# Performance work log

Hardware: AMD Instinct MI355X
Metric: run time of the kernel (lower is better)

## Reference

```python
import jax, jax.numpy as jnp
import numpy as np

N = 500000        # total atoms (n1 nodes)
G = 20000         # graphs (g nodes)
D_IN = 128        # in_features
D_H = 256         # hidden width (config_local / mid_features)
D_OUT = 1         # final output per graph (config_global last int)


def setup_inputs() -> dict:
    key = jax.random.key(0)
    ks = jax.random.split(key, 10)
    h = jax.random.normal(ks[0], (N, D_IN), dtype=jnp.float32)
    graph_ids = jnp.sort(jax.random.randint(ks[1], (N,), 0, G))
    s = 0.05
    return {
        "h": h,
        "graph_ids": graph_ids,
        "num_graphs": G,
        # d_local: Linear(128->256) relu, Linear(256->256) relu
        "W1": jax.random.normal(ks[2], (D_IN, D_H), dtype=jnp.float32) * s,
        "b1": jnp.zeros((D_H,), dtype=jnp.float32),
        "W2": jax.random.normal(ks[3], (D_H, D_H), dtype=jnp.float32) * s,
        "b2": jnp.zeros((D_H,), dtype=jnp.float32),
        # d_global: Linear(256->256) relu, Linear(256->1)
        "Wg1": jax.random.normal(ks[4], (D_H, D_H), dtype=jnp.float32) * s,
        "bg1": jnp.zeros((D_H,), dtype=jnp.float32),
        "Wg2": jax.random.normal(ks[5], (D_H, D_OUT), dtype=jnp.float32) * s,
        "bg2": jnp.zeros((D_OUT,), dtype=jnp.float32),
    }


def reference(h, graph_ids, num_graphs, W1, b1, W2, b2, Wg1, bg1, Wg2, bg2):
    # node-level MLP (d_local): h_global per n1 node
    x = jax.nn.relu(h @ W1 + b1)            # [N, D_H]
    x = jax.nn.relu(x @ W2 + b2)            # [N, D_H]
    # copy_src + sum over n1_in_g edges == per-graph segment sum
    pooled = jax.ops.segment_sum(x, graph_ids, num_segments=num_graphs)  # [G, D_H]
    # graph-level MLP (d_global)
    y = jax.nn.relu(pooled @ Wg1 + bg1)     # [G, D_H]
    return y @ Wg2 + bg2                    # [G, 1]
```

## Files before the change

### kernel.cpp

```cpp
#include <hip/hip_runtime.h>
#include <stdint.h>

#define D_IN 128
#define D_H  256
#define BM   64

typedef float f32x4 __attribute__((ext_vector_type(4)));
typedef short s16x8 __attribute__((ext_vector_type(8)));
typedef unsigned int u32x2 __attribute__((ext_vector_type(2)));
typedef unsigned int u32x4 __attribute__((ext_vector_type(4)));

__device__ __forceinline__ unsigned short f2bf(float x) {
  union { float f; uint32_t u; } v; v.f = x;
  uint32_t r = v.u + 0x7fffu + ((v.u >> 16) & 1u);
  return (unsigned short)(r >> 16);
}
__device__ __forceinline__ float bf2f(unsigned short u) {
  union { uint32_t u; float f; } v; v.u = (uint32_t)u << 16;
  return v.f;
}

__global__ void prep_kernel(const float* __restrict__ W1, const float* __restrict__ W2,
                            const float* __restrict__ Wg1,
                            float* __restrict__ pooled, unsigned short* __restrict__ W1t,
                            unsigned short* __restrict__ W2t, unsigned short* __restrict__ Wg1t,
                            int pooled_n) {
  int stride = gridDim.x * blockDim.x;
  int tid = blockIdx.x * blockDim.x + threadIdx.x;
  for (int i = tid; i < pooled_n; i += stride) pooled[i] = 0.0f;
  for (int i = tid; i < D_H * D_IN; i += stride) {
    int n = i >> 7, k = i & (D_IN - 1);
    W1t[i] = f2bf(W1[k * D_H + n]);
  }
  for (int i = tid; i < D_H * D_H; i += stride) {
    int n = i >> 8, k = i & (D_H - 1);
    W2t[i]  = f2bf(W2[k * D_H + n]);
    Wg1t[i] = f2bf(Wg1[k * D_H + n]);
  }
}


__global__ __launch_bounds__(256, 3)
void node_kernel(const float* __restrict__ h, const int* __restrict__ gids,
                 const float* __restrict__ b1, const float* __restrict__ b2,
                 const unsigned short* __restrict__ W1t, const unsigned short* __restrict__ W2t,
                 float* __restrict__ pooled, int nnodes) {
  __shared__ unsigned short hA[BM * D_IN];
  __shared__ unsigned short x1s[BM * D_H];
  __shared__ int sgid[BM];
  const int tid  = threadIdx.x;
  const int lane = tid & 63;
  const int wave = tid >> 6;
  const int lr   = lane & 15;
  const int q    = lane >> 4;
  const int row0 = blockIdx.x * BM;

  s16x8 a[4][4];
  #pragma unroll
  for (int ks = 0; ks < 4; ++ks)
    #pragma unroll
    for (int mt = 0; mt < 4; ++mt)
      a[ks][mt] = *(const s16x8*)&W1t[(wave * 64 + mt * 16 + lr) * D_IN + ks * 32 + q * 8];

  if (tid < BM) {
    int gr = row0 + tid;
    sgid[tid] = (gr < nnodes) ? gids[gr] : -1;
  }

  #pragma unroll
  for (int i = 0; i < 4; ++i) {
    int gi = tid + i * 256;
    int r  = gi >> 4;
    int gc = gi & 15;
    int gr = row0 + r;
    f32x4 v0 = (f32x4){0.f, 0.f, 0.f, 0.f}, v1 = v0;
    if (gr < nnodes) {
      const f32x4* p = (const f32x4*)(h + (size_t)gr * D_IN + gc * 8);
      v0 = __builtin_nontemporal_load(p);
      v1 = __builtin_nontemporal_load(p + 1);
    }
    u32x4 u;
    u[0] = f2bf(v0[0]) | ((uint32_t)f2bf(v0[1]) << 16);
    u[1] = f2bf(v0[2]) | ((uint32_t)f2bf(v0[3]) << 16);
    u[2] = f2bf(v1[0]) | ((uint32_t)f2bf(v1[1]) << 16);
    u[3] = f2bf(v1[2]) | ((uint32_t)f2bf(v1[3]) << 16);
    *(u32x4*)&hA[r * D_IN + ((gc ^ (r & 7)) << 3)] = u;
  }
  __syncthreads();

  f32x4 acc[4][4];
  #pragma unroll
  for (int mt = 0; mt < 4; ++mt)
    #pragma unroll
    for (int nt = 0; nt < 4; ++nt)
      acc[mt][nt] = (f32x4){0.f, 0.f, 0.f, 0.f};

  #pragma unroll
  for (int ks = 0; ks < 4; ++ks) {
    const int kq = ks * 32 + q * 8;
    s16x8 b[4];
    #pragma unroll
    for (int nt = 0; nt < 4; ++nt)
      b[nt] = *(const s16x8*)&hA[(nt * 16 + lr) * D_IN + (((kq >> 3) ^ (lr & 7)) << 3)];
    #pragma unroll
    for (int mt = 0; mt < 4; ++mt)
      #pragma unroll
      for (int nt = 0; nt < 4; ++nt)
        acc[mt][nt] = __builtin_amdgcn_mfma_f32_16x16x32_bf16(a[ks][mt], b[nt], acc[mt][nt], 0, 0, 0);
  }

  #pragma unroll
  for (int mt = 0; mt < 4; ++mt) {
    int f = wave * 64 + mt * 16 + q * 4;
    float4 bias = *(const float4*)&b1[f];
    #pragma unroll
    for (int nt = 0; nt < 4; ++nt) {
      int nd = nt * 16 + lr;
      uint32_t p0 = f2bf(fmaxf(acc[mt][nt][0] + bias.x, 0.f)) |
                    ((uint32_t)f2bf(fmaxf(acc[mt][nt][1] + bias.y, 0.f)) << 16);
      uint32_t p1 = f2bf(fmaxf(acc[mt][nt][2] + bias.z, 0.f)) |
                    ((uint32_t)f2bf(fmaxf(acc[mt][nt][3] + bias.w, 0.f)) << 16);
      u32x2 w = {p0, p1};
      *(u32x2*)&x1s[nd * D_H + (((f >> 3) ^ (nd & 7)) << 3) + (f & 7)] = w;
    }
  }

  #pragma unroll
  for (int ks = 0; ks < 4; ++ks)
    #pragma unroll
    for (int mt = 0; mt < 4; ++mt)
      a[ks][mt] = *(const s16x8*)&W2t[(wave * 64 + mt * 16 + lr) * D_H + ks * 32 + q * 8];
  __syncthreads();

  #pragma unroll
  for (int mt = 0; mt < 4; ++mt)
    #pragma unroll
    for (int nt = 0; nt < 4; ++nt)
      acc[mt][nt] = (f32x4){0.f, 0.f, 0.f, 0.f};

  #pragma unroll
  for (int ks = 0; ks < 4; ++ks) {
    const int kq = ks * 32 + q * 8;
    s16x8 b[4];
    #pragma unroll
    for (int nt = 0; nt < 4; ++nt)
      b[nt] = *(const s16x8*)&x1s[(nt * 16 + lr) * D_H + (((kq >> 3) ^ (lr & 7)) << 3)];
    #pragma unroll
    for (int mt = 0; mt < 4; ++mt)
      #pragma unroll
      for (int nt = 0; nt < 4; ++nt)
        acc[mt][nt] = __builtin_amdgcn_mfma_f32_16x16x32_bf16(a[ks][mt], b[nt], acc[mt][nt], 0, 0, 0);
  }
  #pragma unroll
  for (int ks = 0; ks < 4; ++ks)
    #pragma unroll
    for (int mt = 0; mt < 4; ++mt)
      a[ks][mt] = *(const s16x8*)&W2t[(wave * 64 + mt * 16 + lr) * D_H + 128 + ks * 32 + q * 8];
  #pragma unroll
  for (int ks = 0; ks < 4; ++ks) {
    const int kq = 128 + ks * 32 + q * 8;
    s16x8 b[4];
    #pragma unroll
    for (int nt = 0; nt < 4; ++nt)
      b[nt] = *(const s16x8*)&x1s[(nt * 16 + lr) * D_H + (((kq >> 3) ^ (lr & 7)) << 3)];
    #pragma unroll
    for (int mt = 0; mt < 4; ++mt)
      #pragma unroll
      for (int nt = 0; nt < 4; ++nt)
        acc[mt][nt] = __builtin_amdgcn_mfma_f32_16x16x32_bf16(a[ks][mt], b[nt], acc[mt][nt], 0, 0, 0);
  }
  __syncthreads();

  #pragma unroll
  for (int mt = 0; mt < 4; ++mt) {
    int f = wave * 64 + mt * 16 + q * 4;
    float4 bias = *(const float4*)&b2[f];
    #pragma unroll
    for (int nt = 0; nt < 4; ++nt) {
      int nd = nt * 16 + lr;
      uint32_t p0 = f2bf(fmaxf(acc[mt][nt][0] + bias.x, 0.f)) |
                    ((uint32_t)f2bf(fmaxf(acc[mt][nt][1] + bias.y, 0.f)) << 16);
      uint32_t p1 = f2bf(fmaxf(acc[mt][nt][2] + bias.z, 0.f)) |
                    ((uint32_t)f2bf(fmaxf(acc[mt][nt][3] + bias.w, 0.f)) << 16);
      u32x2 w = {p0, p1};
      *(u32x2*)&x1s[nd * D_H + (((f >> 3) ^ (nd & 7)) << 3) + (f & 7)] = w;
    }
  }
  __syncthreads();

  float racc = 0.f;
  for (int r = 0; r < BM; ++r) {
    int g = sgid[r];
    if (g >= 0) {
      racc += bf2f(x1s[r * D_H + (((tid >> 3) ^ (r & 7)) << 3) + (tid & 7)]);
      if (r == BM - 1 || sgid[r + 1] != g) {
        atomicAdd(&pooled[g * D_H + tid], racc);
        racc = 0.f;
      }
    }
  }
}

union GraphSmem {
  unsigned short pA[BM][D_H + 8];
  float y[BM][D_H + 4];
};

__global__ __launch_bounds__(256, 2)
void graph_kernel(const float* __restrict__ pooled, const float* __restrict__ bg1,
                  const unsigned short* __restrict__ Wg1t, const float* __restrict__ Wg2,
                  const float* __restrict__ bg2, float* __restrict__ out, int ngraphs) {
  __shared__ GraphSmem sm;
  const int tid  = threadIdx.x;
  const int lane = tid & 63;
  const int wave = tid >> 6;
  const int lr   = lane & 15;
  const int q    = lane >> 4;
  const int g0   = blockIdx.x * BM;

  #pragma unroll
  for (int i = 0; i < 16; ++i) {
    int f4 = tid + i * 256;
    int r  = f4 >> 6;
    int c4 = f4 & 63;
    float4 v = make_float4(0.f, 0.f, 0.f, 0.f);
    if (g0 + r < ngraphs) v = ((const float4*)pooled)[(size_t)(g0 + r) * 64 + c4];
    uint32_t p0 = f2bf(v.x) | ((uint32_t)f2bf(v.y) << 16);
    uint32_t p1 = f2bf(v.z) | ((uint32_t)f2bf(v.w) << 16);
    uint32_t* dst = (uint32_t*)&sm.pA[r][c4 * 4];
    dst[0] = p0; dst[1] = p1;
  }
  __syncthreads();

  f32x4 acc[4][4];
  #pragma unroll
  for (int mt = 0; mt < 4; ++mt)
    #pragma unroll
    for (int nt = 0; nt < 4; ++nt)
      acc[mt][nt] = (f32x4){0.f, 0.f, 0.f, 0.f};

  #pragma unroll
  for (int kk = 0; kk < D_H; kk += 32) {
    const int kq = kk + q * 8;
    s16x8 a[4], b[4];
    #pragma unroll
    for (int mt = 0; mt < 4; ++mt) {
      int f = wave * 64 + mt * 16 + lr;
      a[mt] = *(const s16x8*)&Wg1t[f * D_H + kq];
    }
    #pragma unroll
    for (int nt = 0; nt < 4; ++nt)
      b[nt] = *(const s16x8*)&sm.pA[nt * 16 + lr][kq];
    #pragma unroll
    for (int mt = 0; mt < 4; ++mt)
      #pragma unroll
      for (int nt = 0; nt < 4; ++nt)
        acc[mt][nt] = __builtin_amdgcn_mfma_f32_16x16x32_bf16(a[mt], b[nt], acc[mt][nt], 0, 0, 0);
  }
  __syncthreads();

  #pragma unroll
  for (int mt = 0; mt < 4; ++mt) {
    int f = wave * 64 + mt * 16 + q * 4;
    float4 bias = *(const float4*)&bg1[f];
    #pragma unroll
    for (int nt = 0; nt < 4; ++nt) {
      int nd = nt * 16 + lr;
      f32x4 v;
      v[0] = fmaxf(acc[mt][nt][0] + bias.x, 0.f);
      v[1] = fmaxf(acc[mt][nt][1] + bias.y, 0.f);
      v[2] = fmaxf(acc[mt][nt][2] + bias.z, 0.f);
      v[3] = fmaxf(acc[mt][nt][3] + bias.w, 0.f);
      *(f32x4*)&sm.y[nd][f] = v;
    }
  }
  __syncthreads();

  int gloc = tid >> 2;
  int part = tid & 3;
  float p = 0.f;
  #pragma unroll 8
  for (int i = 0; i < 64; ++i) {
    int f = part + 4 * i;
    p += sm.y[gloc][f] * Wg2[f];
  }
  p += __shfl_xor(p, 1);
  p += __shfl_xor(p, 2);
  if (part == 0 && (g0 + gloc) < ngraphs)
    out[g0 + gloc] = p + bg2[0];
}

extern "C" void kernel_launch(void* const* d_in, const int* in_sizes, int n_in,
                              void* d_out, int out_size, void* d_ws, size_t ws_size,
                              hipStream_t stream) {
  const float* h   = (const float*)d_in[0];
  const int*   gid = (const int*)d_in[1];
  const float* W1  = (const float*)d_in[3];
  const float* b1  = (const float*)d_in[4];
  const float* W2  = (const float*)d_in[5];
  const float* b2  = (const float*)d_in[6];
  const float* Wg1 = (const float*)d_in[7];
  const float* bg1 = (const float*)d_in[8];
  const float* Wg2 = (const float*)d_in[9];
  const float* bg2 = (const float*)d_in[10];
  float* out = (float*)d_out;

  const int N = in_sizes[1];
  const int G = out_size;

  char* ws = (char*)d_ws;
  float* pooled = (float*)ws;
  size_t off = (size_t)G * D_H * sizeof(float);
  unsigned short* W1t  = (unsigned short*)(ws + off); off += (size_t)D_H * D_IN * 2;
  unsigned short* W2t  = (unsigned short*)(ws + off); off += (size_t)D_H * D_H * 2;
  unsigned short* Wg1t = (unsigned short*)(ws + off);

  prep_kernel<<<512, 256, 0, stream>>>(W1, W2, Wg1, pooled, W1t, W2t, Wg1t, G * D_H);
  node_kernel<<<(N + BM - 1) / BM, 256, 0, stream>>>(h, gid, b1, b2, W1t, W2t, pooled, N);
  graph_kernel<<<(G + BM - 1) / BM, 256, 0, stream>>>(pooled, bg1, Wg1t, Wg2, bg2, out, G);
}
```

Before: 579.3 us.

## Make node kernel persistent with double-buffered prefetch of next tile

The node MLP kernel becomes a persistent grid of fixed size that loops over tiles. W1 fragments and biases stay in registers across tiles, and the next tile's h rows and graph ids are prefetched into registers and written to a second LDS buffer while the current tile computes. W2 fragments are streamed in halves to limit register pressure. The graph kernel keeps its intermediate in swizzled bf16 LDS instead of an fp32 union, which allows higher occupancy. The cost is more registers and a lower occupancy bound (2 blocks) for the node kernel, plus bf16 rounding of the graph hidden layer.

```diff
diff --git a/kernel.cpp b/kernel.cpp
--- a/kernel.cpp
+++ b/kernel.cpp
@@ -4,6 +4,7 @@
 #define D_IN 128
 #define D_H  256
 #define BM   64
+#define NODE_GRID 2048
 
 typedef float f32x4 __attribute__((ext_vector_type(4)));
 typedef short s16x8 __attribute__((ext_vector_type(8)));
@@ -27,7 +28,8 @@
                             int pooled_n) {
   int stride = gridDim.x * blockDim.x;
   int tid = blockIdx.x * blockDim.x + threadIdx.x;
-  for (int i = tid; i < pooled_n; i += stride) pooled[i] = 0.0f;
+  float4 z4 = make_float4(0.f, 0.f, 0.f, 0.f);
+  for (int i = tid; i < (pooled_n >> 2); i += stride) ((float4*)pooled)[i] = z4;
   for (int i = tid; i < D_H * D_IN; i += stride) {
     int n = i >> 7, k = i & (D_IN - 1);
     W1t[i] = f2bf(W1[k * D_H + n]);
@@ -39,52 +41,249 @@
   }
 }
 
-
-__global__ __launch_bounds__(256, 3)
+__global__ __launch_bounds__(256, 2)
 void node_kernel(const float* __restrict__ h, const int* __restrict__ gids,
                  const float* __restrict__ b1, const float* __restrict__ b2,
                  const unsigned short* __restrict__ W1t, const unsigned short* __restrict__ W2t,
-                 float* __restrict__ pooled, int nnodes) {
-  __shared__ unsigned short hA[BM * D_IN];
+                 float* __restrict__ pooled, int nnodes, int ntiles) {
+  __shared__ unsigned short hA[2][BM * D_IN];
   __shared__ unsigned short x1s[BM * D_H];
-  __shared__ int sgid[BM];
+  __shared__ int sgid[2][BM];
   const int tid  = threadIdx.x;
   const int lane = tid & 63;
   const int wave = tid >> 6;
   const int lr   = lane & 15;
   const int q    = lane >> 4;
-  const int row0 = blockIdx.x * BM;
-
-  s16x8 a[4][4];
+
+  if (blockIdx.x >= ntiles) return;
+
+  s16x8 a1[4][4];
   #pragma unroll
   for (int ks = 0; ks < 4; ++ks)
     #pragma unroll
     for (int mt = 0; mt < 4; ++mt)
-      a[ks][mt] = *(const s16x8*)&W1t[(wave * 64 + mt * 16 + lr) * D_IN + ks * 32 + q * 8];
-
-  if (tid < BM) {
-    int gr = row0 + tid;
-    sgid[tid] = (gr < nnodes) ? gids[gr] : -1;
-  }
-
-  #pragma unroll
-  for (int i = 0; i < 4; ++i) {
-    int gi = tid + i * 256;
-    int r  = gi >> 4;
-    int gc = gi & 15;
-    int gr = row0 + r;
+      a1[ks][mt] = *(const s16x8*)&W1t[(wave * 64 + mt * 16 + lr) * D_IN + ks * 32 + q * 8];
+  float4 b1v[4], b2v[4];
+  #pragma unroll
+  for (int mt = 0; mt < 4; ++mt) {
+    b1v[mt] = *(const float4*)&b1[wave * 64 + mt * 16 + q * 4];
+    b2v[mt] = *(const float4*)&b2[wave * 64 + mt * 16 + q * 4];
+  }
+
+  int tile = blockIdx.x;
+
+  {
+    const int row0 = tile * BM;
+    #pragma unroll
+    for (int i = 0; i < 4; ++i) {
+      int gi = tid + i * 256, r = gi >> 4, gc = gi & 15, gr = row0 + r;
+      f32x4 v0 = (f32x4){0.f, 0.f, 0.f, 0.f}, v1 = v0;
+      if (gr < nnodes) {
+        const f32x4* p = (const f32x4*)(h + (size_t)gr * D_IN + gc * 8);
+        v0 = __builtin_nontemporal_load(p);
+        v1 = __builtin_nontemporal_load(p + 1);
+      }
+      u32x4 u;
+      u[0] = f2bf(v0[0]) | ((uint32_t)f2bf(v0[1]) << 16);
+      u[1] = f2bf(v0[2]) | ((uint32_t)f2bf(v0[3]) << 16);
+      u[2] = f2bf(v1[0]) | ((uint32_t)f2bf(v1[1]) << 16);
+      u[3] = f2bf(v1[2]) | ((uint32_t)f2bf(v1[3]) << 16);
+      *(u32x4*)&hA[0][r * D_IN + ((gc ^ (r & 7)) << 3)] = u;
+    }
+    if (tid < BM) {
+      int gr = row0 + tid;
+      sgid[0][tid] = (gr < nnodes) ? gids[gr] : -1;
+    }
+  }
+  __syncthreads();
+
+  auto body = [&](int cur) {
+    const int nxt = cur ^ 1;
+    const int ntile = tile + NODE_GRID;
+    const bool has_next = ntile < ntiles;
+    const int nrow0 = ntile * BM;
+
+    f32x4 hv[8];
+    #pragma unroll
+    for (int i = 0; i < 4; ++i) {
+      int gi = tid + i * 256, r = gi >> 4, gc = gi & 15;
+      int gr = nrow0 + r;
+      hv[2 * i] = (f32x4){0.f, 0.f, 0.f, 0.f};
+      hv[2 * i + 1] = hv[2 * i];
+      if (has_next && gr < nnodes) {
+        const f32x4* p = (const f32x4*)(h + (size_t)gr * D_IN + gc * 8);
+        hv[2 * i]     = __builtin_nontemporal_load(p);
+        hv[2 * i + 1] = __builtin_nontemporal_load(p + 1);
+      }
+    }
+    int gv = -1;
+    if (has_next && tid < BM) {
+      int gr = nrow0 + tid;
+      gv = (gr < nnodes) ? gids[gr] : -1;
+    }
+
+    f32x4 acc[4][4];
+    #pragma unroll
+    for (int mt = 0; mt < 4; ++mt)
+      #pragma unroll
+      for (int nt = 0; nt < 4; ++nt)
+        acc[mt][nt] = (f32x4){0.f, 0.f, 0.f, 0.f};
+
+    #pragma unroll
+    for (int ks = 0; ks < 4; ++ks) {
+      const int kq = ks * 32 + q * 8;
+      s16x8 b[4];
+      #pragma unroll
+      for (int nt = 0; nt < 4; ++nt)
+        b[nt] = *(const s16x8*)&hA[cur][(nt * 16 + lr) * D_IN + (((kq >> 3) ^ (lr & 7)) << 3)];
+      #pragma unroll
+      for (int mt = 0; mt < 4; ++mt)
+        #pragma unroll
+        for (int nt = 0; nt < 4; ++nt)
+          acc[mt][nt] = __builtin_amdgcn_mfma_f32_16x16x32_bf16(a1[ks][mt], b[nt], acc[mt][nt], 0, 0, 0);
+    }
+
+    #pragma unroll
+    for (int mt = 0; mt < 4; ++mt) {
+      int f = wave * 64 + mt * 16 + q * 4;
+      #pragma unroll
+      for (int nt = 0; nt < 4; ++nt) {
+        int nd = nt * 16 + lr;
+        uint32_t p0 = f2bf(fmaxf(acc[mt][nt][0] + b1v[mt].x, 0.f)) |
+                      ((uint32_t)f2bf(fmaxf(acc[mt][nt][1] + b1v[mt].y, 0.f)) << 16);
+        uint32_t p1 = f2bf(fmaxf(acc[mt][nt][2] + b1v[mt].z, 0.f)) |
+                      ((uint32_t)f2bf(fmaxf(acc[mt][nt][3] + b1v[mt].w, 0.f)) << 16);
+        u32x2 w = {p0, p1};
+        *(u32x2*)&x1s[nd * D_H + (((f >> 3) ^ (nd & 7)) << 3) + (f & 7)] = w;
+      }
+    }
+
+    if (has_next) {
+      #pragma unroll
+      for (int i = 0; i < 4; ++i) {
+        int gi = tid + i * 256, r = gi >> 4, gc = gi & 15;
+        u32x4 u;
+        u[0] = f2bf(hv[2 * i][0]) | ((uint32_t)f2bf(hv[2 * i][1]) << 16);
+        u[1] = f2bf(hv[2 * i][2]) | ((uint32_t)f2bf(hv[2 * i][3]) << 16);
+        u[2] = f2bf(hv[2 * i + 1][0]) | ((uint32_t)f2bf(hv[2 * i + 1][1]) << 16);
+        u[3] = f2bf(hv[2 * i + 1][2]) | ((uint32_t)f2bf(hv[2 * i + 1][3]) << 16);
+        *(u32x4*)&hA[nxt][r * D_IN + ((gc ^ (r & 7)) << 3)] = u;
+      }
+    }
+
+    s16x8 w2[2][2][4];
+    #pragma unroll
+    for (int qq = 0; qq < 2; ++qq)
+      #pragma unroll
+      for (int ki = 0; ki < 2; ++ki)
+        #pragma unroll
+        for (int mt = 0; mt < 4; ++mt)
+          w2[qq][ki][mt] = *(const s16x8*)&W2t[(wave * 64 + mt * 16 + lr) * D_H +
+                                               ((qq * 2 + ki) * 32 + q * 8)];
+
+    __syncthreads();
+
+    #pragma unroll
+    for (int mt = 0; mt < 4; ++mt)
+      #pragma unroll
+      for (int nt = 0; nt < 4; ++nt)
+        acc[mt][nt] = (f32x4){0.f, 0.f, 0.f, 0.f};
+
+    #pragma unroll
+    for (int qq = 0; qq < 4; ++qq) {
+      const int buf = qq & 1;
+      #pragma unroll
+      for (int ki = 0; ki < 2; ++ki) {
+        const int kq = (qq * 2 + ki) * 32 + q * 8;
+        s16x8 b[4];
+        #pragma unroll
+        for (int nt = 0; nt < 4; ++nt)
+          b[nt] = *(const s16x8*)&x1s[(nt * 16 + lr) * D_H + (((kq >> 3) ^ (lr & 7)) << 3)];
+        #pragma unroll
+        for (int mt = 0; mt < 4; ++mt)
+          #pragma unroll
+          for (int nt = 0; nt < 4; ++nt)
+            acc[mt][nt] = __builtin_amdgcn_mfma_f32_16x16x32_bf16(w2[buf][ki][mt], b[nt], acc[mt][nt], 0, 0, 0);
+      }
+      if (qq < 2) {
+        #pragma unroll
+        for (int ki = 0; ki < 2; ++ki)
+          #pragma unroll
+          for (int mt = 0; mt < 4; ++mt)
+            w2[buf][ki][mt] = *(const s16x8*)&W2t[(wave * 64 + mt * 16 + lr) * D_H +
+                                                  (((qq + 2) * 2 + ki) * 32 + q * 8)];
+      }
+    }
+
+    __syncthreads();
+
+    if (has_next && tid < BM) sgid[nxt][tid] = gv;
+
+    #pragma unroll
+    for (int mt = 0; mt < 4; ++mt) {
+      int f = wave * 64 + mt * 16 + q * 4;
+      #pragma unroll
+      for (int nt = 0; nt < 4; ++nt) {
+        int nd = nt * 16 + lr;
+        uint32_t p0 = f2bf(fmaxf(acc[mt][nt][0] + b2v[mt].x, 0.f)) |
+                      ((uint32_t)f2bf(fmaxf(acc[mt][nt][1] + b2v[mt].y, 0.f)) << 16);
+        uint32_t p1 = f2bf(fmaxf(acc[mt][nt][2] + b2v[mt].z, 0.f)) |
+                      ((uint32_t)f2bf(fmaxf(acc[mt][nt][3] + b2v[mt].w, 0.f)) << 16);
+        u32x2 w = {p0, p1};
+        *(u32x2*)&x1s[nd * D_H + (((f >> 3) ^ (nd & 7)) << 3) + (f & 7)] = w;
+      }
+    }
+
+    float racc = 0.f;
+    for (int r = 0; r < BM; ++r) {
+      int g = sgid[cur][r];
+      if (g >= 0) {
+        racc += bf2f(x1s[r * D_H + (((tid >> 3) ^ (r & 7)) << 3) + (tid & 7)]);
+        if (r == BM - 1 || sgid[cur][r + 1] != g) {
+          atomicAdd(&pooled[g * D_H + tid], racc);
+          racc = 0.f;
+        }
+      }
+    }
+  };
+
+  while (true) {
+    body(0);
+    tile += NODE_GRID;
+    if (tile >= ntiles) break;
+    body(1);
+    tile += NODE_GRID;
+    if (tile >= ntiles) break;
+  }
+}
+
+__global__ __launch_bounds__(256, 4)
+void graph_kernel(const float* __restrict__ pooled, const float* __restrict__ bg1,
+                  const unsigned short* __restrict__ Wg1t, const float* __restrict__ Wg2,
+                  const float* __restrict__ bg2, float* __restrict__ out, int ngraphs) {
+  __shared__ unsigned short pA[BM * D_H];
+  const int tid  = threadIdx.x;
+  const int lane = tid & 63;
+  const int wave = tid >> 6;
+  const int lr   = lane & 15;
+  const int q    = lane >> 4;
+  const int g0   = blockIdx.x * BM;
+
+  #pragma unroll
+  for (int i = 0; i < 8; ++i) {
+    int gi = tid + i * 256, r = gi >> 5, gc = gi & 31;
+    int gr = g0 + r;
     f32x4 v0 = (f32x4){0.f, 0.f, 0.f, 0.f}, v1 = v0;
-    if (gr < nnodes) {
-      const f32x4* p = (const f32x4*)(h + (size_t)gr * D_IN + gc * 8);
-      v0 = __builtin_nontemporal_load(p);
-      v1 = __builtin_nontemporal_load(p + 1);
+    if (gr < ngraphs) {
+      const f32x4* p = (const f32x4*)(pooled + (size_t)gr * D_H + gc * 8);
+      v0 = p[0]; v1 = p[1];
     }
     u32x4 u;
     u[0] = f2bf(v0[0]) | ((uint32_t)f2bf(v0[1]) << 16);
     u[1] = f2bf(v0[2]) | ((uint32_t)f2bf(v0[3]) << 16);
     u[2] = f2bf(v1[0]) | ((uint32_t)f2bf(v1[1]) << 16);
     u[3] = f2bf(v1[2]) | ((uint32_t)f2bf(v1[3]) << 16);
-    *(u32x4*)&hA[r * D_IN + ((gc ^ (r & 7)) << 3)] = u;
+    *(u32x4*)&pA[r * D_H + (((gc & 7) ^ (r & 7)) << 3) + ((gc & 24) << 3)] = u;
   }
   __syncthreads();
 
@@ -96,23 +295,29 @@
       acc[mt][nt] = (f32x4){0.f, 0.f, 0.f, 0.f};
 
   #pragma unroll
-  for (int ks = 0; ks < 4; ++ks) {
+  for (int ks = 0; ks < 8; ++ks) {
     const int kq = ks * 32 + q * 8;
-    s16x8 b[4];
-    #pragma unroll
-    for (int nt = 0; nt < 4; ++nt)
-      b[nt] = *(const s16x8*)&hA[(nt * 16 + lr) * D_IN + (((kq >> 3) ^ (lr & 7)) << 3)];
+    s16x8 a[4], b[4];
+    #pragma unroll
+    for (int mt = 0; mt < 4; ++mt)
+      a[mt] = *(const s16x8*)&Wg1t[(wave * 64 + mt * 16 + lr) * D_H + kq];
+    #pragma unroll
+    for (int nt = 0; nt < 4; ++nt) {
+      int row = nt * 16 + lr, gw = kq >> 3;
+      b[nt] = *(const s16x8*)&pA[row * D_H + (((gw & 7) ^ (row & 7)) << 3) + ((gw & 24) << 3)];
+    }
     #pragma unroll
     for (int mt = 0; mt < 4; ++mt)
       #pragma unroll
       for (int nt = 0; nt < 4; ++nt)
-        acc[mt][nt] = __builtin_amdgcn_mfma_f32_16x16x32_bf16(a[ks][mt], b[nt], acc[mt][nt], 0, 0, 0);
-  }
+        acc[mt][nt] = __builtin_amdgcn_mfma_f32_16x16x32_bf16(a[mt], b[nt], acc[mt][nt], 0, 0, 0);
+  }
+  __syncthreads();
 
   #pragma unroll
   for (int mt = 0; mt < 4; ++mt) {
     int f = wave * 64 + mt * 16 + q * 4;
-    float4 bias = *(const float4*)&b1[f];
+    float4 bias = *(const float4*)&bg1[f];
     #pragma unroll
     for (int nt = 0; nt < 4; ++nt) {
       int nd = nt * 16 + lr;
@@ -121,157 +326,8 @@
       uint32_t p1 = f2bf(fmaxf(acc[mt][nt][2] + bias.z, 0.f)) |
                     ((uint32_t)f2bf(fmaxf(acc[mt][nt][3] + bias.w, 0.f)) << 16);
       u32x2 w = {p0, p1};
-      *(u32x2*)&x1s[nd * D_H + (((f >> 3) ^ (nd & 7)) << 3) + (f & 7)] = w;
-    }
-  }
-
-  #pragma unroll
-  for (int ks = 0; ks < 4; ++ks)
-    #pragma unroll
-    for (int mt = 0; mt < 4; ++mt)
-      a[ks][mt] = *(const s16x8*)&W2t[(wave * 64 + mt * 16 + lr) * D_H + ks * 32 + q * 8];
-  __syncthreads();
-
-  #pragma unroll
-  for (int mt = 0; mt < 4; ++mt)
-    #pragma unroll
-    for (int nt = 0; nt < 4; ++nt)
-      acc[mt][nt] = (f32x4){0.f, 0.f, 0.f, 0.f};
-
-  #pragma unroll
-  for (int ks = 0; ks < 4; ++ks) {
-    const int kq = ks * 32 + q * 8;
-    s16x8 b[4];
-    #pragma unroll
-    for (int nt = 0; nt < 4; ++nt)
-      b[nt] = *(const s16x8*)&x1s[(nt * 16 + lr) * D_H + (((kq >> 3) ^ (lr & 7)) << 3)];
-    #pragma unroll
-    for (int mt = 0; mt < 4; ++mt)
-      #pragma unroll
-      for (int nt = 0; nt < 4; ++nt)
-        acc[mt][nt] = __builtin_amdgcn_mfma_f32_16x16x32_bf16(a[ks][mt], b[nt], acc[mt][nt], 0, 0, 0);
-  }
-  #pragma unroll
-  for (int ks = 0; ks < 4; ++ks)
-    #pragma unroll
-    for (int mt = 0; mt < 4; ++mt)
-      a[ks][mt] = *(const s16x8*)&W2t[(wave * 64 + mt * 16 + lr) * D_H + 128 + ks * 32 + q * 8];
-  #pragma unroll
-  for (int ks = 0; ks < 4; ++ks) {
-    const int kq = 128 + ks * 32 + q * 8;
-    s16x8 b[4];
-    #pragma unroll
-    for (int nt = 0; nt < 4; ++nt)
-      b[nt] = *(const s16x8*)&x1s[(nt * 16 + lr) * D_H + (((kq >> 3) ^ (lr & 7)) << 3)];
-    #pragma unroll
-    for (int mt = 0; mt < 4; ++mt)
-      #pragma unroll
-      for (int nt = 0; nt < 4; ++nt)
-        acc[mt][nt] = __builtin_amdgcn_mfma_f32_16x16x32_bf16(a[ks][mt], b[nt], acc[mt][nt], 0, 0, 0);
-  }
-  __syncthreads();
-
-  #pragma unroll
-  for (int mt = 0; mt < 4; ++mt) {
-    int f = wave * 64 + mt * 16 + q * 4;
-    float4 bias = *(const float4*)&b2[f];
-    #pragma unroll
-    for (int nt = 0; nt < 4; ++nt) {
-      int nd = nt * 16 + lr;
-      uint32_t p0 = f2bf(fmaxf(acc[mt][nt][0] + bias.x, 0.f)) |
-                    ((uint32_t)f2bf(fmaxf(acc[mt][nt][1] + bias.y, 0.f)) << 16);
-      uint32_t p1 = f2bf(fmaxf(acc[mt][nt][2] + bias.z, 0.f)) |
-                    ((uint32_t)f2bf(fmaxf(acc[mt][nt][3] + bias.w, 0.f)) << 16);
-      u32x2 w = {p0, p1};
-      *(u32x2*)&x1s[nd * D_H + (((f >> 3) ^ (nd & 7)) << 3) + (f & 7)] = w;
-    }
-  }
-  __syncthreads();
-
-  float racc = 0.f;
-  for (int r = 0; r < BM; ++r) {
-    int g = sgid[r];
-    if (g >= 0) {
-      racc += bf2f(x1s[r * D_H + (((tid >> 3) ^ (r & 7)) << 3) + (tid & 7)]);
-      if (r == BM - 1 || sgid[r + 1] != g) {
-        atomicAdd(&pooled[g * D_H + tid], racc);
-        racc = 0.f;
-      }
-    }
-  }
-}
-
-union GraphSmem {
-  unsigned short pA[BM][D_H + 8];
-  float y[BM][D_H + 4];
-};
-
-__global__ __launch_bounds__(256, 2)
-void graph_kernel(const float* __restrict__ pooled, const float* __restrict__ bg1,
-                  const unsigned short* __restrict__ Wg1t, const float* __restrict__ Wg2,
-                  const float* __restrict__ bg2, float* __restrict__ out, int ngraphs) {
-  __shared__ GraphSmem sm;
-  const int tid  = threadIdx.x;
-  const int lane = tid & 63;
-  const int wave = tid >> 6;
-  const int lr   = lane & 15;
-  const int q    = lane >> 4;
-  const int g0   = blockIdx.x * BM;
-
-  #pragma unroll
-  for (int i = 0; i < 16; ++i) {
-    int f4 = tid + i * 256;
-    int r  = f4 >> 6;
-    int c4 = f4 & 63;
-    float4 v = make_float4(0.f, 0.f, 0.f, 0.f);
-    if (g0 + r < ngraphs) v = ((const float4*)pooled)[(size_t)(g0 + r) * 64 + c4];
-    uint32_t p0 = f2bf(v.x) | ((uint32_t)f2bf(v.y) << 16);
-    uint32_t p1 = f2bf(v.z) | ((uint32_t)f2bf(v.w) << 16);
-    uint32_t* dst = (uint32_t*)&sm.pA[r][c4 * 4];
-    dst[0] = p0; dst[1] = p1;
-  }
-  __syncthreads();
-
-  f32x4 acc[4][4];
-  #pragma unroll
-  for (int mt = 0; mt < 4; ++mt)
-    #pragma unroll
-    for (int nt = 0; nt < 4; ++nt)
-      acc[mt][nt] = (f32x4){0.f, 0.f, 0.f, 0.f};
-
-  #pragma unroll
-  for (int kk = 0; kk < D_H; kk += 32) {
-    const int kq = kk + q * 8;
-    s16x8 a[4], b[4];
-    #pragma unroll
-    for (int mt = 0; mt < 4; ++mt) {
-      int f = wave * 64 + mt * 16 + lr;
-      a[mt] = *(const s16x8*)&Wg1t[f * D_H + kq];
-    }
-    #pragma unroll
-    for (int nt = 0; nt < 4; ++nt)
-      b[nt] = *(const s16x8*)&sm.pA[nt * 16 + lr][kq];
-    #pragma unroll
-    for (int mt = 0; mt < 4; ++mt)
-      #pragma unroll
-      for (int nt = 0; nt < 4; ++nt)
-        acc[mt][nt] = __builtin_amdgcn_mfma_f32_16x16x32_bf16(a[mt], b[nt], acc[mt][nt], 0, 0, 0);
-  }
-  __syncthreads();
-
-  #pragma unroll
-  for (int mt = 0; mt < 4; ++mt) {
-    int f = wave * 64 + mt * 16 + q * 4;
-    float4 bias = *(const float4*)&bg1[f];
-    #pragma unroll
-    for (int nt = 0; nt < 4; ++nt) {
-      int nd = nt * 16 + lr;
-      f32x4 v;
-      v[0] = fmaxf(acc[mt][nt][0] + bias.x, 0.f);
-      v[1] = fmaxf(acc[mt][nt][1] + bias.y, 0.f);
-      v[2] = fmaxf(acc[mt][nt][2] + bias.z, 0.f);
-      v[3] = fmaxf(acc[mt][nt][3] + bias.w, 0.f);
-      *(f32x4*)&sm.y[nd][f] = v;
+      int gw = f >> 3;
+      *(u32x2*)&pA[nd * D_H + (((gw & 7) ^ (nd & 7)) << 3) + ((gw & 24) << 3) + (f & 7)] = w;
     }
   }
   __syncthreads();
@@ -280,9 +336,15 @@
   int part = tid & 3;
   float p = 0.f;
   #pragma unroll 8
-  for (int i = 0; i < 64; ++i) {
-    int f = part + 4 * i;
-    p += sm.y[gloc][f] * Wg2[f];
+  for (int i = 0; i < 32; ++i) {
+    int f2 = part + 4 * i;
+    int hw = 2 * f2;
+    int gw = hw >> 3;
+    uint32_t wv = *(const uint32_t*)&pA[gloc * D_H + (((gw & 7) ^ (gloc & 7)) << 3) +
+                                        ((gw & 24) << 3) + (hw & 7)];
+    float2 wg = ((const float2*)Wg2)[f2];
+    p += bf2f((unsigned short)(wv & 0xffffu)) * wg.x +
+         bf2f((unsigned short)(wv >> 16)) * wg.y;
   }
   p += __shfl_xor(p, 1);
   p += __shfl_xor(p, 2);
@@ -307,6 +369,7 @@
 
   const int N = in_sizes[1];
   const int G = out_size;
+  const int ntiles = (N + BM - 1) / BM;
 
   char* ws = (char*)d_ws;
   float* pooled = (float*)ws;
@@ -316,6 +379,6 @@
   unsigned short* Wg1t = (unsigned short*)(ws + off);
 
   prep_kernel<<<512, 256, 0, stream>>>(W1, W2, Wg1, pooled, W1t, W2t, Wg1t, G * D_H);
-  node_kernel<<<(N + BM - 1) / BM, 256, 0, stream>>>(h, gid, b1, b2, W1t, W2t, pooled, N);
+  node_kernel<<<NODE_GRID, 256, 0, stream>>>(h, gid, b1, b2, W1t, W2t, pooled, N, ntiles);
   graph_kernel<<<(G + BM - 1) / BM, 256, 0, stream>>>(pooled, bg1, Wg1t, Wg2, bg2, out, G);
 }
```

Result: slower. 809.0 us (+39.6%).
